# Kernel tuning notes

Measured on AMD Instinct MI355X. Metric: run time of the kernel, lower is better.

Reference implementation:

```python
import jax, jax.numpy as jnp
import numpy as np

WS = 8          # window size
SHIFT = 4       # shift size
NH = 16         # num heads
K_RATE = 0.75
N_WIN = WS * WS # tokens per window = 64
TOPK = max(1, int(N_WIN * K_RATE))  # 48
EPS = 1e-5


def _rel_pos_index(ws):
    coords = np.stack(np.meshgrid(np.arange(ws), np.arange(ws), indexing='ij'))  # (2,ws,ws)
    cf = coords.reshape(2, -1)
    rel = (cf[:, :, None] - cf[:, None, :]).transpose(1, 2, 0).astype(np.int64)
    rel[:, :, 0] += ws - 1
    rel[:, :, 1] += ws - 1
    rel[:, :, 0] *= 2 * ws - 1
    return rel.sum(-1)  # (N,N)


def _attn_mask(H, W, ws, shift):
    img = np.zeros((H, W))
    sl = (slice(0, -ws), slice(-ws, -shift), slice(-shift, None))
    cnt = 0
    for hs in sl:
        for wsl in sl:
            img[hs, wsl] = cnt
            cnt += 1
    mw = img.reshape(H // ws, ws, W // ws, ws).transpose(0, 2, 1, 3).reshape(-1, ws * ws)
    am = mw[:, None, :] - mw[:, :, None]
    return np.where(am != 0, -100.0, 0.0).astype(np.float32)  # (nW,N,N)


def _win_part(x, ws):
    B, H, W, C = x.shape
    x = x.reshape(B, H // ws, ws, W // ws, ws, C).transpose(0, 1, 3, 2, 4, 5)
    return x.reshape(-1, ws * ws, C)


def _win_rev(w, ws, H, W, B, C):
    x = w.reshape(B, H // ws, W // ws, ws, ws, C).transpose(0, 1, 3, 2, 4, 5)
    return x.reshape(B, H, W, C)


def _ln(x, g, b):
    m = jnp.mean(x, -1, keepdims=True)
    v = jnp.var(x, -1, keepdims=True)
    return (x - m) * jax.lax.rsqrt(v + EPS) * g + b


def setup_inputs() -> dict:
    key = jax.random.key(0)
    ks = jax.random.split(key, 16)
    B, H, W, C = 16, 64, 64, 512
    hid = int(C * 4.0)
    s = lambda k, shp: jax.random.normal(k, shp, dtype=jnp.float32) * 0.02
    return {
        'x': jax.random.normal(ks[0], (B, H * W, C), dtype=jnp.float32),
        'norm1_g': jnp.ones((C,), jnp.float32), 'norm1_b': jnp.zeros((C,), jnp.float32),
        'qkv_w': s(ks[1], (C, 3 * C)), 'qkv_b': jnp.zeros((3 * C,), jnp.float32),
        'rel_bias': s(ks[2], ((2 * WS - 1) * (2 * WS - 1), NH)),
        'proj_w': s(ks[3], (C, C)), 'proj_b': jnp.zeros((C,), jnp.float32),
        'norm2_g': jnp.ones((C,), jnp.float32), 'norm2_b': jnp.zeros((C,), jnp.float32),
        'fc1_w': s(ks[4], (C, hid)), 'fc1_b': jnp.zeros((hid,), jnp.float32),
        'fc2_w': s(ks[5], (hid, C)), 'fc2_b': jnp.zeros((C,), jnp.float32),
    }


def reference(x, norm1_g, norm1_b, qkv_w, qkv_b, rel_bias, proj_w, proj_b,
              norm2_g, norm2_b, fc1_w, fc1_b, fc2_w, fc2_b):
    B, L, C = x.shape
    H = W = 64
    hd = C // NH
    scale = hd ** -0.5
    rpi = _rel_pos_index(WS)                      # (N,N) int, trace-time constant
    amask = jnp.asarray(_attn_mask(H, W, WS, SHIFT))  # (nW,N,N)
    nW = amask.shape[0]

    shortcut = x
    y = _ln(x, norm1_g, norm1_b).reshape(B, H, W, C)
    y = jnp.roll(y, shift=(-SHIFT, -SHIFT), axis=(1, 2))
    xw = _win_part(y, WS)                         # (Bw, N, C), Bw = B*nW
    Bw, N, _ = xw.shape

    qkv = (xw @ qkv_w + qkv_b).reshape(Bw, N, 3, NH, hd).transpose(2, 0, 3, 1, 4)
    q, k, v = qkv[0] * scale, qkv[1], qkv[2]      # (Bw,NH,N,hd)
    attn = jnp.einsum('bhnd,bhmd->bhnm', q, k)    # (Bw,NH,N,N)
    bias = rel_bias[rpi.reshape(-1)].reshape(N, N, NH).transpose(2, 0, 1)
    attn = attn + bias[None]
    # faithful to source: masked_fill(mask > 0, -inf); mask values are {-100,0} -> no-op
    m = jnp.broadcast_to(amask[None, :, None], (B, nW, NH, N, N)).reshape(Bw, NH, N, N)
    attn = jnp.where(m > 0, -jnp.inf, attn)

    vals, idx = jax.lax.top_k(attn, TOPK)         # (Bw,NH,N,K)
    w = jax.nn.softmax(vals, axis=-1)
    # gather top-k V rows: flatten (N,K) for a single take_along_axis
    v_g = jnp.take_along_axis(v, idx.reshape(Bw, NH, N * TOPK)[..., None], axis=2)
    v_g = v_g.reshape(Bw, NH, N, TOPK, hd)
    out = jnp.einsum('bhnk,bhnkd->bhnd', w, v_g)  # (Bw,NH,N,hd)
    out = out.transpose(0, 2, 1, 3).reshape(Bw, N, C)
    out = out @ proj_w + proj_b

    sx = _win_rev(out.reshape(-1, WS, WS, C), WS, H, W, B, C)
    sx = jnp.roll(sx, shift=(SHIFT, SHIFT), axis=(1, 2)).reshape(B, L, C)
    x = shortcut + sx
    h = _ln(x, norm2_g, norm2_b)
    h = jax.nn.gelu(h @ fc1_w + fc1_b, approximate=False) @ fc2_w + fc2_b
    return x + h
```

## Files before the change

kernel.cpp:

```cpp
#include <hip/hip_runtime.h>
#include <stdint.h>

typedef __attribute__((ext_vector_type(8))) short short8;
typedef __attribute__((ext_vector_type(4))) float floatx4;

__device__ __forceinline__ float bf2f(unsigned short h) {
  union { unsigned int u; float f; } v; v.u = ((unsigned int)h) << 16; return v.f;
}
__device__ __forceinline__ unsigned short f2bf(float f) {
  union { float f; unsigned int u; } v; v.f = f;
  unsigned int r = v.u + 0x7fffu + ((v.u >> 16) & 1u);
  return (unsigned short)(r >> 16);
}

__device__ __forceinline__ void gll16(const void* g, void* l) {
  __builtin_amdgcn_global_load_lds((const __attribute__((address_space(1))) unsigned int*)g,
                                   (__attribute__((address_space(3))) unsigned int*)l, 16, 0, 0);
}

template <int K>
__device__ __forceinline__ float rorf(float x) {
  return __int_as_float(__builtin_amdgcn_update_dpp(0, __float_as_int(x), 0x120 + K, 0xF, 0xF, false));
}
__device__ __forceinline__ float grpsum16(float v) {
  v += rorf<1>(v); v += rorf<2>(v); v += rorf<4>(v); v += rorf<8>(v);
  return v;
}
__device__ __forceinline__ float swz16(float x) {
  return __int_as_float(__builtin_amdgcn_ds_swizzle(__float_as_int(x), 0x401F));
}

__global__ __launch_bounds__(256) void transpose_kern(const float* __restrict__ in,
                                                      unsigned short* __restrict__ out,
                                                      int K, int N) {
  __shared__ float tile[32][33];
  const int tx = threadIdx.x & 31, ty = threadIdx.x >> 5;
  const int n0 = blockIdx.x * 32, k0 = blockIdx.y * 32;
#pragma unroll
  for (int i = 0; i < 4; ++i)
    tile[ty + 8 * i][tx] = in[(size_t)(k0 + ty + 8 * i) * N + n0 + tx];
  __syncthreads();
#pragma unroll
  for (int i = 0; i < 4; ++i)
    out[(size_t)(n0 + ty + 8 * i) * K + k0 + tx] = f2bf(tile[tx][ty + 8 * i]);
}

template <int BF16IN>
__global__ __launch_bounds__(256) void ln_kern(const void* __restrict__ xv,
                                               const float* __restrict__ g,
                                               const float* __restrict__ b,
                                               unsigned short* __restrict__ out,
                                               int tokenBase, int scatter) {
  const int t = tokenBase + blockIdx.x;
  const int c = threadIdx.x * 2;
  float x0, x1;
  if (BF16IN) {
    const unsigned int u = *(const unsigned int*)((const unsigned short*)xv + (size_t)t * 512 + c);
    x0 = bf2f((unsigned short)(u & 0xffffu)); x1 = bf2f((unsigned short)(u >> 16));
  } else {
    const float* xr = (const float*)xv + (size_t)t * 512;
    x0 = xr[c]; x1 = xr[c + 1];
  }
  float s = x0 + x1, s2 = x0 * x0 + x1 * x1;
#pragma unroll
  for (int off = 32; off; off >>= 1) {
    s += __shfl_xor(s, off, 64);
    s2 += __shfl_xor(s2, off, 64);
  }
  __shared__ float red[2][4];
  const int l = threadIdx.x & 63, wv = threadIdx.x >> 6;
  if (l == 0) { red[0][wv] = s; red[1][wv] = s2; }
  __syncthreads();
  s = red[0][0] + red[0][1] + red[0][2] + red[0][3];
  s2 = red[1][0] + red[1][1] + red[1][2] + red[1][3];
  const float mean = s * (1.0f / 512.0f);
  const float var = s2 * (1.0f / 512.0f) - mean * mean;
  const float rstd = rsqrtf(var + 1e-5f);
  const float y0 = (x0 - mean) * rstd * g[c] + b[c];
  const float y1 = (x1 - mean) * rstd * g[c + 1] + b[c + 1];
  int orow;
  if (scatter) {
    const int bb = t >> 12, rem = t & 4095, h = rem >> 6, w = rem & 63;
    const int hp = (h + 60) & 63, wp = (w + 60) & 63;
    const int wh = hp >> 3, i = hp & 7, ww = wp >> 3, j = wp & 7;
    const int rg = ((bb << 6) + (wh << 3) + ww) * 64 + (i << 3) + j;
    orow = rg - tokenBase;
  } else {
    orow = blockIdx.x;
  }
  const unsigned int o = (unsigned int)f2bf(y0) | ((unsigned int)f2bf(y1) << 16);
  *(unsigned int*)(out + (size_t)orow * 512 + c) = o;
}

template <int EPI>
__global__ __launch_bounds__(256) void gemm_bt(const unsigned short* __restrict__ A,
                                               const unsigned short* __restrict__ Bt,
                                               const float* __restrict__ bias,
                                               void* __restrict__ outv,
                                               const void* __restrict__ resv,
                                               int M, int N, int K, int rowBase) {
  __shared__ unsigned short As[2][128][64];
  __shared__ unsigned short Bs[2][128][64];
  const int tid = threadIdx.x;
  const int l = tid & 63, wv = tid >> 6;
  const int wm = wv >> 1, wn = wv & 1;
  const int bm = blockIdx.y * 128, bn = blockIdx.x * 128;

  floatx4 acc[4][4];
#pragma unroll
  for (int i = 0; i < 4; ++i)
#pragma unroll
    for (int j = 0; j < 4; ++j) acc[i][j] = {0.0f, 0.0f, 0.0f, 0.0f};

  const int srow = l >> 3;
  const int sslot = ((l & 7) ^ (l >> 3)) * 8;
  const unsigned short* Abase = A + (size_t)(bm + srow) * K + sslot;
  const unsigned short* Bbase = Bt + (size_t)(bn + srow) * K + sslot;

#define STAGE(bb, k0)                                                        \
  {                                                                          \
    _Pragma("unroll")                                                        \
    for (int tt = 0; tt < 4; ++tt) {                                         \
      const int r = wv * 32 + tt * 8;                                        \
      gll16(Abase + (size_t)r * K + (k0), &As[bb][r][0]);                    \
      gll16(Bbase + (size_t)r * K + (k0), &Bs[bb][r][0]);                    \
    }                                                                        \
  }

  STAGE(0, 0);
  __syncthreads();

  const int ntl = K >> 6;
  int cur = 0;
#pragma unroll 1
  for (int t = 0; t < ntl; ++t) {
    if (t + 1 < ntl) STAGE(cur ^ 1, (t + 1) * 64);
#pragma unroll
    for (int kh = 0; kh < 2; ++kh) {
      const int rslot = ((kh * 4 + (l >> 4)) ^ (l & 7)) * 8;
      short8 af[4], bfr[4];
#pragma unroll
      for (int mt = 0; mt < 4; ++mt)
        af[mt] = *(const short8*)&As[cur][wm * 64 + mt * 16 + (l & 15)][rslot];
#pragma unroll
      for (int nt2 = 0; nt2 < 4; ++nt2)
        bfr[nt2] = *(const short8*)&Bs[cur][wn * 64 + nt2 * 16 + (l & 15)][rslot];
#pragma unroll
      for (int mt = 0; mt < 4; ++mt)
#pragma unroll
        for (int nt2 = 0; nt2 < 4; ++nt2)
          acc[mt][nt2] = __builtin_amdgcn_mfma_f32_16x16x32_bf16(af[mt], bfr[nt2], acc[mt][nt2], 0, 0, 0);
    }
    if (t + 1 < ntl) {
      __syncthreads();
      cur ^= 1;
    }
  }
#undef STAGE

#pragma unroll
  for (int mt = 0; mt < 4; ++mt) {
#pragma unroll
    for (int nt2 = 0; nt2 < 4; ++nt2) {
      const int gcol = bn + wn * 64 + nt2 * 16 + (l & 15);
      const float bv = bias[gcol];
#pragma unroll
      for (int r = 0; r < 4; ++r) {
        const int grow = bm + wm * 64 + mt * 16 + (l >> 4) * 4 + r;
        float v = acc[mt][nt2][r] + bv;
        if (EPI == 2) {
          const int rg = rowBase + grow;
          const int bw = rg >> 6, n = rg & 63;
          const int bb = bw >> 6, wi = bw & 63;
          const int i = n >> 3, j = n & 7;
          const int hp = ((wi >> 3) << 3) + i;
          const int wp = ((wi & 7) << 3) + j;
          const int h = (hp + 4) & 63, w = (wp + 4) & 63;
          const size_t t = (size_t)((bb << 12) + (h << 6) + w);
          ((unsigned short*)outv)[t * 512 + gcol] = f2bf(v + ((const float*)resv)[t * 512 + gcol]);
        } else if (EPI == 3) {
          ((float*)outv)[(size_t)grow * 512 + gcol] =
              v + bf2f(((const unsigned short*)resv)[(size_t)grow * 512 + gcol]);
        } else {
          ((unsigned short*)outv)[(size_t)grow * (size_t)N + gcol] = f2bf(v);
        }
      }
    }
  }
}

template <int EPI>
__global__ __launch_bounds__(512) void gemm256(const unsigned short* __restrict__ A,
                                               const unsigned short* __restrict__ Bt,
                                               const float* __restrict__ bias,
                                               unsigned short* __restrict__ out,
                                               int M, int N, int K) {
  __shared__ unsigned short As[2][256][64];
  __shared__ unsigned short Bs[2][256][64];
  const int tid = threadIdx.x;
  const int l = tid & 63, wid = tid >> 6;
  const int wm = wid >> 2, wn = wid & 3;
  const int bm = blockIdx.y * 256, bn = blockIdx.x * 256;

  floatx4 acc[8][4];
#pragma unroll
  for (int i = 0; i < 8; ++i)
#pragma unroll
    for (int j = 0; j < 4; ++j) acc[i][j] = {0.0f, 0.0f, 0.0f, 0.0f};

  const int srow = tid >> 3;
  const int sslot = ((tid & 7) ^ (srow & 7)) * 8;
  const unsigned short* Ab = A + (size_t)(bm + srow) * K + sslot;
  const unsigned short* Bb = Bt + (size_t)(bn + srow) * K + sslot;
  const int ldsbase = wid * 8;

#define STG256(bb, k0)                                                          \
  {                                                                             \
    _Pragma("unroll")                                                           \
    for (int tt = 0; tt < 4; ++tt) {                                            \
      gll16(Ab + (size_t)(tt * 64) * K + (k0), &As[bb][tt * 64 + ldsbase][0]);  \
      gll16(Bb + (size_t)(tt * 64) * K + (k0), &Bs[bb][tt * 64 + ldsbase][0]);  \
    }                                                                           \
  }

  STG256(0, 0);
  __syncthreads();

  const int ntl = K >> 6;
  int cur = 0;
#pragma unroll 1
  for (int t = 0; t < ntl; ++t) {
    if (t + 1 < ntl) STG256(cur ^ 1, (t + 1) * 64);
#pragma unroll
    for (int kh = 0; kh < 2; ++kh) {
      const int rslot = ((kh * 4 + (l >> 4)) ^ (l & 7)) * 8;
      short8 af[8], bfr[4];
#pragma unroll
      for (int mt = 0; mt < 8; ++mt)
        af[mt] = *(const short8*)&As[cur][wm * 128 + mt * 16 + (l & 15)][rslot];
#pragma unroll
      for (int nt2 = 0; nt2 < 4; ++nt2)
        bfr[nt2] = *(const short8*)&Bs[cur][wn * 64 + nt2 * 16 + (l & 15)][rslot];
#pragma unroll
      for (int mt = 0; mt < 8; ++mt)
#pragma unroll
        for (int nt2 = 0; nt2 < 4; ++nt2)
          acc[mt][nt2] = __builtin_amdgcn_mfma_f32_16x16x32_bf16(af[mt], bfr[nt2], acc[mt][nt2], 0, 0, 0);
    }
    if (t + 1 < ntl) {
      __syncthreads();
      cur ^= 1;
    }
  }
#undef STG256

#pragma unroll
  for (int mt = 0; mt < 8; ++mt) {
#pragma unroll
    for (int nt2 = 0; nt2 < 4; ++nt2) {
      const int gcol = bn + wn * 64 + nt2 * 16 + (l & 15);
      const float bv = bias[gcol];
#pragma unroll
      for (int r = 0; r < 4; ++r) {
        const int grow = bm + wm * 128 + mt * 16 + (l >> 4) * 4 + r;
        float v = acc[mt][nt2][r] + bv;
        if (EPI == 1) {
          const float t2 = v * (1.5957691216057308f + 0.071354816222f * v * v);
          v = v * (1.0f / (1.0f + __expf(-t2)));
        }
        out[(size_t)grow * (size_t)N + gcol] = f2bf(v);
      }
    }
  }
}

__global__ __launch_bounds__(512) void attn_kern(const unsigned short* __restrict__ qkv,
                                                 const float* __restrict__ relb,
                                                 unsigned short* __restrict__ attnout) {
  __shared__ float Ss[64][66];
  __shared__ unsigned short VT[32][66];
  __shared__ float biasL[240];

  const int u = blockIdx.x;
  const int bwl = u >> 4, head = u & 15;
  const int tid = threadIdx.x;
  const int l = tid & 63, w = tid >> 6;

  if (tid < 256) {
    const int row = tid >> 2, d0 = (tid & 3) * 8;
    short8 v8 = *(const short8*)(qkv + (size_t)(bwl * 64 + row) * 1536 + 1024 + head * 32 + d0);
#pragma unroll
    for (int j = 0; j < 8; ++j) VT[d0 + j][row] = (unsigned short)v8[j];
  } else if (tid < 256 + 225) {
    biasL[tid - 256] = relb[(tid - 256) * 16 + head];
  }
  __syncthreads();

  {
    const int rb = w >> 1, ch = w & 1;
    short8 a = *(const short8*)(qkv + (size_t)(bwl * 64 + rb * 16 + (l & 15)) * 1536 +
                                head * 32 + (l >> 4) * 8);
    const int n0 = rb * 16 + (l >> 4) * 4;
    const int m0 = ch * 32 + (l & 15);
    const int ibase = ((n0 >> 3) - (m0 >> 3) + 7) * 15 + ((n0 & 7) - (m0 & 7) + 7);
#pragma unroll
    for (int nt2 = 0; nt2 < 2; ++nt2) {
      short8 bfr = *(const short8*)(qkv + (size_t)(bwl * 64 + ch * 32 + nt2 * 16 + (l & 15)) * 1536 +
                                    512 + head * 32 + (l >> 4) * 8);
      floatx4 z = {0.0f, 0.0f, 0.0f, 0.0f};
      floatx4 d = __builtin_amdgcn_mfma_f32_16x16x32_bf16(a, bfr, z, 0, 0, 0);
#pragma unroll
      for (int r = 0; r < 4; ++r)
        Ss[n0 + r][m0 + nt2 * 16] = fmaf(d[r], 0.17677669529663689f, biasL[ibase + r - 30 * nt2]);
    }
  }
  __syncthreads();

  float* srow_base = &Ss[w * 8][0];
#pragma unroll 1
  for (int rr = 0; rr < 8; ++rr) {
    const float own = srow_base[rr * 66 + l];
    const unsigned int uo = __float_as_uint(own);
    const unsigned int mapped = uo ^ ((unsigned int)((int)uo >> 31) | 0x80000000u);
    unsigned int p = 0;
#pragma unroll 1
    for (int b = 31; b >= 0; --b) {
      const unsigned int cand = p | (1u << b);
      const int c = __popcll(__ballot(mapped >= cand));
      if (c >= 48) {
        p = cand;
        if (c == 48) break;
      }
    }
    const float tf = __uint_as_float((p & 0x80000000u) ? (p ^ 0x80000000u) : ~p);
    const float e = (mapped >= p) ? __expf(own - tf) : 0.0f;
    float zs = grpsum16(e);
    zs += swz16(zs);
    zs += __shfl_xor(zs, 32, 64);
    ((unsigned short*)(srow_base + rr * 66))[l] = f2bf(e * __builtin_amdgcn_rcpf(zs));
  }
  __syncthreads();

  {
    const int rb = w >> 1, cb = w & 1;
    floatx4 acc = {0.0f, 0.0f, 0.0f, 0.0f};
#pragma unroll
    for (int kh = 0; kh < 2; ++kh) {
      short8 pa = *(const short8*)((const unsigned short*)&Ss[rb * 16 + (l & 15)][0] +
                                   kh * 32 + (l >> 4) * 8);
      short8 vb = *(const short8*)&VT[cb * 16 + (l & 15)][kh * 32 + (l >> 4) * 8];
      acc = __builtin_amdgcn_mfma_f32_16x16x32_bf16(pa, vb, acc, 0, 0, 0);
    }
#pragma unroll
    for (int r = 0; r < 4; ++r) {
      const int n = rb * 16 + (l >> 4) * 4 + r;
      const int dcol = cb * 16 + (l & 15);
      attnout[(size_t)(bwl * 64 + n) * 512 + head * 32 + dcol] = f2bf(acc[r]);
    }
  }
}

extern "C" void kernel_launch(void* const* d_in, const int* in_sizes, int n_in,
                              void* d_out, int out_size, void* d_ws, size_t ws_size,
                              hipStream_t stream) {
  (void)in_sizes; (void)n_in; (void)out_size;
  const float* x      = (const float*)d_in[0];
  const float* n1g    = (const float*)d_in[1];
  const float* n1b    = (const float*)d_in[2];
  const float* qkv_w  = (const float*)d_in[3];
  const float* qkv_b  = (const float*)d_in[4];
  const float* relb   = (const float*)d_in[5];
  const float* proj_w = (const float*)d_in[6];
  const float* proj_b = (const float*)d_in[7];
  const float* n2g    = (const float*)d_in[8];
  const float* n2b    = (const float*)d_in[9];
  const float* fc1_w  = (const float*)d_in[10];
  const float* fc1_b  = (const float*)d_in[11];
  const float* fc2_w  = (const float*)d_in[12];
  const float* fc2_b  = (const float*)d_in[13];
  float* outp = (float*)d_out;

  unsigned short* qkvT  = (unsigned short*)d_ws;
  unsigned short* projT = qkvT + 1536 * 512;
  unsigned short* fc1T  = projT + 512 * 512;
  unsigned short* fc2T  = fc1T + 2048 * 512;
  const size_t wbytes = (size_t)(1536 * 512 + 512 * 512 + 2048 * 512 + 512 * 2048) * 2;
  unsigned short* x2bf = (unsigned short*)((char*)d_ws + wbytes);
  const size_t x2bytes = (size_t)65536 * 512 * 2;
  size_t rem = (ws_size > wbytes + x2bytes) ? ws_size - wbytes - x2bytes : 0;
  int R = (int)(rem / 5120);
  R = (R / 4096) * 4096;
  if (R > 65536) R = 65536;
  if (R < 4096) R = 4096;
  const int nch = 65536 / R;
  unsigned short* bufA = x2bf + (size_t)65536 * 512;
  unsigned short* bufB = bufA + (size_t)R * 512;

  transpose_kern<<<dim3(1536 / 32, 512 / 32), 256, 0, stream>>>(qkv_w, qkvT, 512, 1536);
  transpose_kern<<<dim3(512 / 32, 512 / 32), 256, 0, stream>>>(proj_w, projT, 512, 512);
  transpose_kern<<<dim3(2048 / 32, 512 / 32), 256, 0, stream>>>(fc1_w, fc1T, 512, 2048);
  transpose_kern<<<dim3(512 / 32, 2048 / 32), 256, 0, stream>>>(fc2_w, fc2T, 2048, 512);

  for (int cb = 0; cb < nch; ++cb) {
    ln_kern<0><<<R, 256, 0, stream>>>(x, n1g, n1b, bufA, cb * R, 1);
    gemm_bt<0><<<dim3(12, R / 128), 256, 0, stream>>>(bufA, qkvT, qkv_b, bufB, nullptr,
                                                      R, 1536, 512, 0);
    attn_kern<<<(R / 64) * 16, 512, 0, stream>>>(bufB, relb, bufA);
    gemm_bt<2><<<dim3(4, R / 128), 256, 0, stream>>>(bufA, projT, proj_b, x2bf, x,
                                                     R, 512, 512, cb * R);
    ln_kern<1><<<R, 256, 0, stream>>>(x2bf, n2g, n2b, bufA, cb * R, 0);
    gemm256<1><<<dim3(2048 / 256, R / 256), 512, 0, stream>>>(bufA, fc1T, fc1_b, bufB,
                                                              R, 2048, 512);
    gemm_bt<3><<<dim3(4, R / 128), 256, 0, stream>>>(bufB, fc2T, fc2_b,
                                                     outp + (size_t)cb * R * 512,
                                                     x2bf + (size_t)cb * R * 512,
                                                     R, 512, 2048, 0);
  }
}
```

Baseline: 1.041 ms.

## Use 256x256 GEMM tiles for QKV and FC2 with XCD-aware block remapping

Adds an XCD-aware swizzle of workgroup ids so that blocks sharing A/B tiles land on the same chiplet's L2. It also routes the QKV and FC2 GEMMs through the larger 256x256-tile kernel, which gains a residual-add fp32 epilogue, with the 128-tile kernel kept as a fallback. The aim is better L2 locality and more operand reuse per loaded tile. FC2 at 256 tiles launches only 2 x R/256 blocks, which may leave CUs underused when R is small.

```diff
diff --git a/kernel.cpp b/kernel.cpp
--- a/kernel.cpp
+++ b/kernel.cpp
@@ -16,6 +16,17 @@
 __device__ __forceinline__ void gll16(const void* g, void* l) {
   __builtin_amdgcn_global_load_lds((const __attribute__((address_space(1))) unsigned int*)g,
                                    (__attribute__((address_space(3))) unsigned int*)l, 16, 0, 0);
+}
+
+__device__ __forceinline__ int xcd_swz_id() {
+  const int nx = gridDim.x;
+  const int nwg = nx * gridDim.y;
+  const int orig = blockIdx.y * nx + blockIdx.x;
+  if ((nwg & 7) == 0) {
+    const int q = nwg >> 3;
+    return (orig & 7) * q + (orig >> 3);
+  }
+  return orig;
 }
 
 template <int K>
@@ -104,7 +115,8 @@
   const int tid = threadIdx.x;
   const int l = tid & 63, wv = tid >> 6;
   const int wm = wv >> 1, wn = wv & 1;
-  const int bm = blockIdx.y * 128, bn = blockIdx.x * 128;
+  const int id = xcd_swz_id();
+  const int bm = (id / gridDim.x) * 128, bn = (id % gridDim.x) * 128;
 
   floatx4 acc[4][4];
 #pragma unroll
@@ -193,14 +205,16 @@
 __global__ __launch_bounds__(512) void gemm256(const unsigned short* __restrict__ A,
                                                const unsigned short* __restrict__ Bt,
                                                const float* __restrict__ bias,
-                                               unsigned short* __restrict__ out,
+                                               void* __restrict__ outv,
+                                               const void* __restrict__ resv,
                                                int M, int N, int K) {
   __shared__ unsigned short As[2][256][64];
   __shared__ unsigned short Bs[2][256][64];
   const int tid = threadIdx.x;
   const int l = tid & 63, wid = tid >> 6;
   const int wm = wid >> 2, wn = wid & 3;
-  const int bm = blockIdx.y * 256, bn = blockIdx.x * 256;
+  const int id = xcd_swz_id();
+  const int bm = (id / gridDim.x) * 256, bn = (id % gridDim.x) * 256;
 
   floatx4 acc[8][4];
 #pragma unroll
@@ -268,7 +282,12 @@
           const float t2 = v * (1.5957691216057308f + 0.071354816222f * v * v);
           v = v * (1.0f / (1.0f + __expf(-t2)));
         }
-        out[(size_t)grow * (size_t)N + gcol] = f2bf(v);
+        if (EPI == 3) {
+          ((float*)outv)[(size_t)grow * 512 + gcol] =
+              v + bf2f(((const unsigned short*)resv)[(size_t)grow * 512 + gcol]);
+        } else {
+          ((unsigned short*)outv)[(size_t)grow * (size_t)N + gcol] = f2bf(v);
+        }
       }
     }
   }
@@ -403,17 +422,31 @@
 
   for (int cb = 0; cb < nch; ++cb) {
     ln_kern<0><<<R, 256, 0, stream>>>(x, n1g, n1b, bufA, cb * R, 1);
-    gemm_bt<0><<<dim3(12, R / 128), 256, 0, stream>>>(bufA, qkvT, qkv_b, bufB, nullptr,
-                                                      R, 1536, 512, 0);
+    if ((R & 255) == 0) {
+      gemm256<0><<<dim3(6, R / 256), 512, 0, stream>>>(bufA, qkvT, qkv_b, bufB, nullptr,
+                                                       R, 1536, 512);
+    } else {
+      gemm_bt<0><<<dim3(12, R / 128), 256, 0, stream>>>(bufA, qkvT, qkv_b, bufB, nullptr,
+                                                        R, 1536, 512, 0);
+    }
     attn_kern<<<(R / 64) * 16, 512, 0, stream>>>(bufB, relb, bufA);
     gemm_bt<2><<<dim3(4, R / 128), 256, 0, stream>>>(bufA, projT, proj_b, x2bf, x,
                                                      R, 512, 512, cb * R);
     ln_kern<1><<<R, 256, 0, stream>>>(x2bf, n2g, n2b, bufA, cb * R, 0);
-    gemm256<1><<<dim3(2048 / 256, R / 256), 512, 0, stream>>>(bufA, fc1T, fc1_b, bufB,
-                                                              R, 2048, 512);
-    gemm_bt<3><<<dim3(4, R / 128), 256, 0, stream>>>(bufB, fc2T, fc2_b,
-                                                     outp + (size_t)cb * R * 512,
-                                                     x2bf + (size_t)cb * R * 512,
-                                                     R, 512, 2048, 0);
-  }
-}
+    if ((R & 255) == 0) {
+      gemm256<1><<<dim3(8, R / 256), 512, 0, stream>>>(bufA, fc1T, fc1_b, bufB, nullptr,
+                                                       R, 2048, 512);
+      gemm256<3><<<dim3(2, R / 256), 512, 0, stream>>>(bufB, fc2T, fc2_b,
+                                                       outp + (size_t)cb * R * 512,
+                                                       x2bf + (size_t)cb * R * 512,
+                                                       R, 512, 2048);
+    } else {
+      gemm_bt<1><<<dim3(16, R / 128), 256, 0, stream>>>(bufA, fc1T, fc1_b, bufB, nullptr,
+                                                        R, 2048, 512, 0);
+      gemm_bt<3><<<dim3(4, R / 128), 256, 0, stream>>>(bufB, fc2T, fc2_b,
+                                                       outp + (size_t)cb * R * 512,
+                                                       x2bf + (size_t)cb * R * 512,
+                                                       R, 512, 2048, 0);
+    }
+  }
+}
```

After: 936.1 us. 1.11x faster.
